# Kernel tuning notes

Measured on AMD Instinct MI355X. Metric: run time of the kernel, lower is better.

The kernel has to match this reference:

```python
import jax, jax.numpy as jnp
import numpy as np

B, H, W = 1024, 66, 64
N = 62          # EEG channels / graph nodes
TOPK = 62       # hardcoded in Network
NUM_CLASSES = 3


def setup_inputs() -> dict:
    key = jax.random.key(0)
    ks = jax.random.split(key, 17)
    p = lambda i, s: (jax.random.normal(ks[i], s, jnp.float32) * 0.05)
    return {
        "x": jax.random.normal(ks[0], (B, H, W), jnp.float32),
        "conv_w": p(1, (32, 1, 5, 5)), "conv_b": p(2, (32,)),
        "s1_bn_w": p(3, (480, 64)), "s1_bn_b": p(4, (64,)),
        "s1_g_w": p(5, (480, 32)), "s1_g_b": p(6, (32,)),
        "s2_bn_w": p(7, (32, 64)), "s2_bn_b": p(8, (64,)),
        "s2_g_w": p(9, (32, 32)), "s2_g_b": p(10, (32,)),
        "s3_bn_w": p(11, (32, 64)), "s3_bn_b": p(12, (64,)),
        "s3_g_w": p(13, (32, 32)), "s3_g_b": p(14, (32,)),
        "fc_w": p(15, (620, NUM_CLASSES)), "fc_b": p(16, (NUM_CLASSES,)),
    }


def _maxpool_last(x, k):
    # MaxPool over the last dim with kernel=stride=k, VALID (floor) semantics.
    win = (1,) * (x.ndim - 1) + (k,)
    return jax.lax.reduce_window(x, -jnp.inf, jax.lax.max, win, win, "VALID")


def _sogc(x, bn_w, bn_b, g_w, g_b):
    # x: (Bg, N, F). Self-organized graph construction + DenseGCNConv.
    Bg = x.shape[0]
    xa = jnp.tanh(x @ bn_w + bn_b)                     # (Bg, N, bn)
    adj = jax.nn.softmax(jnp.einsum("bnf,bmf->bnm", xa, xa), axis=2)
    # topk mask per row (scatter of ones at top-k column indices)
    _, idx = jax.lax.top_k(adj, TOPK)                  # (Bg, N, k)
    bi = jnp.arange(Bg)[:, None, None]
    ri = jnp.arange(N)[None, :, None]
    mask = jnp.zeros_like(adj).at[bi, ri, idx].set(1.0)
    adj = adj * mask
    # SOGC adds eye, then DenseGCNConv(add_loop=True) overwrites diag with 1
    d = jnp.arange(N)
    adj = adj.at[:, d, d].set(1.0)
    # symmetric degree normalization with clamp(min=1)
    deg_is = jnp.clip(adj.sum(-1), 1.0, None) ** -0.5  # (Bg, N)
    adj = deg_is[:, :, None] * adj * deg_is[:, None, :]
    return jnp.einsum("bnm,bmo->bno", adj, x @ g_w) + g_b


def reference(x, conv_w, conv_b, s1_bn_w, s1_bn_b, s1_g_w, s1_g_b,
              s2_bn_w, s2_bn_b, s2_g_w, s2_g_b,
              s3_bn_w, s3_bn_b, s3_g_w, s3_g_b, fc_w, fc_b):
    b = x.shape[0]
    h = jax.lax.conv_general_dilated(
        x[:, None], conv_w, (1, 1), "VALID",
        dimension_numbers=("NCHW", "OIHW", "NCHW"))
    h = jax.nn.relu(h + conv_b[None, :, None, None])   # (B,32,62,60)
    h = _maxpool_last(h, 4)                            # (B,32,62,15)
    h = h.reshape(b, -1, 480)                          # (B,62,480)
    h = _sogc(h.reshape(-1, N, 480), s1_bn_w, s1_bn_b, s1_g_w, s1_g_b)
    h = _sogc(h.reshape(-1, N, 32), s2_bn_w, s2_bn_b, s2_g_w, s2_g_b)
    h = _sogc(h.reshape(-1, N, 32), s3_bn_w, s3_bn_b, s3_g_w, s3_g_b)
    h = _maxpool_last(h, 3)                            # (B,62,10)
    h = h.reshape(h.shape[0], -1)                      # (B,620) — adapted head
    return h @ fc_w + fc_b                             # (B,3)
```

## Files before the change

### kernel.cpp

```cpp
#include <hip/hip_runtime.h>
#include <math.h>


typedef _Float16 f16x8 __attribute__((ext_vector_type(8)));
typedef float    f32x4  __attribute__((ext_vector_type(4)));
typedef float    f32x16 __attribute__((ext_vector_type(16)));

__device__ __forceinline__ unsigned short f32_to_f16u(float f) {
    const _Float16 h = (_Float16)f;
    return __builtin_bit_cast(unsigned short, h);
}
__device__ __forceinline__ float f16u_to_f32(unsigned short u) {
    return (float)__builtin_bit_cast(_Float16, u);
}
__device__ __forceinline__ float fast_tanh(float v) {
    v = fminf(fmaxf(v, -15.f), 15.f);
    const float ex = __expf(2.f * v);
    return (ex - 1.f) / (ex + 1.f);
}


__global__ __launch_bounds__(256) void prepack_kernel(
    const float* __restrict__ bnw1, const float* __restrict__ gw1,
    const float* __restrict__ cw,
    const float* __restrict__ bnw2, const float* __restrict__ gw2,
    const float* __restrict__ bnw3, const float* __restrict__ gw3,
    unsigned short* __restrict__ wp)
{
    const int idx = blockIdx.x * 256 + threadIdx.x;
    if (idx < 49152) {
        const int kc = idx / 3072, r = idx - kc * 3072;
        const int q = r / 768, r2 = r - q * 768;
        const int col = r2 >> 3, j = r2 & 7;
        float w = 0.f;
        if (kc < 15) {
            const int s = q * 8 + j;
            const int ko = s * 15 + kc;
            w = (col < 64) ? bnw1[ko * 64 + col] : gw1[ko * 32 + (col - 64)];
        }
        wp[idx] = f32_to_f16u(w);
    } else if (idx >= 92160 && idx < 93696) {
        const int e = idx - 92160;
        const int c = e >> 9, l = (e >> 3) & 63, j = e & 7;
        const int ch = l & 31, dio = l >> 5;
        const int di = (c < 2) ? (2 * c + dio) : (4 + dio);
        const float w = (j < 5 && di < 5) ? cw[ch * 25 + di * 5 + j] : 0.f;
        wp[idx] = f32_to_f16u(w);
    } else if (idx >= 94208 && idx < 100352) {
        const int e2 = idx - 94208;
        const int s = e2 / 3072, r = e2 - s * 3072;
        const int col = r >> 5, k = r & 31;
        const float* bnw = s ? bnw3 : bnw2;
        const float* gw  = s ? gw3  : gw2;
        const float w = (col < 64) ? bnw[k * 64 + col] : gw[k * 32 + (col - 64)];
        wp[idx] = f32_to_f16u(w);
    }
}

__global__ __launch_bounds__(256, 4) void mega_kernel(
    const float* __restrict__ x,
    const float* __restrict__ cb,
    const unsigned short* __restrict__ wp,
    const float* __restrict__ bnb1,  const float* __restrict__ gb1,
    const float* __restrict__ bnb2,  const float* __restrict__ gb2,
    const float* __restrict__ bnb3,  const float* __restrict__ gb3,
    const float* __restrict__ fcw,   const float* __restrict__ fcb,
    float* __restrict__ out)
{
    __shared__ __align__(16) char lds[28416];
    unsigned short* xb   = (unsigned short*)lds;
    unsigned short* Xcol = (unsigned short*)(lds + 10880);
    unsigned short* xaH  = (unsigned short*)lds;
    unsigned short* zB   = xaH + 4608;
    unsigned short* P    = xaH + 6912;
    unsigned short* xB   = xaH + 11520;
    float* degis = (float*)(lds + 28160);

    const int b = blockIdx.x;
    const int tid = threadIdx.x;
    const int wv = tid >> 6, ln = tid & 63;

    const float4* xg = (const float4*)(x + (size_t)b * 4224);
    for (int idx = tid; idx < 1056; idx += 256) {
        const float4 v = xg[idx];
        const int row = idx >> 4, c4 = idx & 15;
        short4 s;
        s.x = (short)f32_to_f16u(v.x);
        s.y = (short)f32_to_f16u(v.y);
        s.z = (short)f32_to_f16u(v.z);
        s.w = (short)f32_to_f16u(v.w);
        *(short4*)(xb + row * 80 + c4 * 4) = s;
    }
    for (int idx = tid; idx < 544; idx += 256) {
        const int row = idx >> 3, w = idx & 7;
        ((unsigned int*)(xb + row * 80 + 64))[w] = 0u;
    }
    if (tid < 64) {
        const int row = 66 + (tid >> 5), w = tid & 31;
        ((unsigned int*)(xb + row * 80))[w] = 0u;
    }
    if (tid < 128)
        ((unsigned int*)(Xcol + 62 * 128))[tid] = 0u;
    __syncthreads();

    const int m = ln & 15, rp = (ln >> 4) & 1, dio = ln >> 5;
    const int ch = ln & 31, hi = ln >> 5;
    f16x8 Wc[3];
    #pragma unroll
    for (int c = 0; c < 3; ++c)
        Wc[c] = *(const f16x8*)(wp + 92160 + c * 512 + ln * 8);
    const float cbv = cb[ch];
    const f32x16 z16 = {};

    const int rt = ln & 15, q = ln >> 4;
    f32x4 acc[6];
    #pragma unroll
    for (int nt = 0; nt < 6; ++nt) acc[nt] = (f32x4){0.f, 0.f, 0.f, 0.f};

    for (int pjg = 0; pjg < 4; ++pjg) {
        const int j0 = pjg * 16;
        f16x8 Bp[6];
        {
            const unsigned short* wB = wp + (pjg * 4) * 3072 + q * 768 + rt * 8;
            #pragma unroll
            for (int nt = 0; nt < 6; ++nt) Bp[nt] = *(const f16x8*)(wB + nt * 128);
        }
        #pragma unroll 4
        for (int p = wv; p < 31; p += 4) {
            const int r0 = 2 * p;
            const unsigned short* base = xb + (r0 + rp + dio) * 80 + j0 + m;
            f32x16 a32;
            #pragma unroll
            for (int c = 0; c < 3; ++c) {
                const f16x8 Af = *(const f16x8*)(base + c * 160);
                a32 = __builtin_amdgcn_mfma_f32_32x32x16_f16(
                          Af, Wc[c], (c == 0) ? z16 : a32, 0, 0, 0);
            }
            #pragma unroll
            for (int i = 0; i < 4; ++i) {
                const int t = 2 * i + hi;
                const int rpo = t >> 2, g = t & 3;
                float v = fmaxf(fmaxf(a32[4 * i], a32[4 * i + 1]),
                                fmaxf(a32[4 * i + 2], a32[4 * i + 3])) + cbv;
                v = fmaxf(v, 0.f);
                if (!(pjg == 3 && g == 3)) {
                    const int row = r0 + rpo;
                    const int tt = ch * 62 + row;
                    const int n = tt >> 5, sf = tt & 31;
                    Xcol[n * 128 + ((g * 32 + sf) ^ ((n & 7) << 3))] =
                        f32_to_f16u(v);
                }
            }
        }
        __syncthreads();
        {
            const int row = wv * 16 + rt;
            #pragma unroll
            for (int g = 0; g < 4; ++g) {
                f16x8 Bn[6];
                #pragma unroll
                for (int nt = 0; nt < 6; ++nt)
                    Bn[nt] = (g < 3)
                        ? *(const f16x8*)(wp + (pjg * 4 + g + 1) * 3072
                                          + q * 768 + nt * 128 + rt * 8)
                        : Bp[nt];
                const f16x8 A = *(const f16x8*)(
                    Xcol + row * 128 + (((g * 4 + q) ^ (row & 7)) << 3));
                #pragma unroll
                for (int nt = 0; nt < 6; ++nt)
                    acc[nt] = __builtin_amdgcn_mfma_f32_16x16x32_f16(A, Bp[nt], acc[nt], 0, 0, 0);
                #pragma unroll
                for (int nt = 0; nt < 6; ++nt) Bp[nt] = Bn[nt];
            }
        }
        __syncthreads();
    }

    {
        const int rq = wv * 4 + q;
        #pragma unroll
        for (int nt = 0; nt < 4; ++nt) {
            const float bb = bnb1[nt * 16 + rt];
            #pragma unroll
            for (int j = 0; j < 4; ++j) {
                const int r = rq * 4 + j;
                float th = fast_tanh(acc[nt][j] + bb);
                if (r >= 62) th = 0.f;
                xaH[r * 72 + nt * 16 + rt] = f32_to_f16u(th);
            }
        }
        #pragma unroll
        for (int nt = 4; nt < 6; ++nt) {
            const int o = (nt - 4) * 16 + rt;
            unsigned short zv[4];
            #pragma unroll
            for (int j = 0; j < 4; ++j) {
                const int r = rq * 4 + j;
                zv[j] = (r < 62) ? f32_to_f16u(acc[nt][j]) : (unsigned short)0;
            }
            *(ushort4*)(zB + o * 72 + rq * 4) =
                make_ushort4(zv[0], zv[1], zv[2], zv[3]);
        }
    }
    __syncthreads();

    const int c16 = ln & 15;
    const int r62 = wv * 16 + c16;
    const unsigned short* wstg = wp + 94208;

    #pragma unroll 1
    for (int st = 0; st < 3; ++st) {
        f16x8 zPre[2][2];
        #pragma unroll
        for (int kh = 0; kh < 2; ++kh) {
            const int chh = (kh * 4 + q) * 8;
            zPre[kh][0] = *(const f16x8*)(zB + c16 * 72 + chh);
            zPre[kh][1] = *(const f16x8*)(zB + (16 + c16) * 72 + chh);
        }
        f32x4 sacc[4];
        #pragma unroll
        for (int ct = 0; ct < 4; ++ct) sacc[ct] = (f32x4){0.f, 0.f, 0.f, 0.f};
        const int arow = r62 * 72;
        #pragma unroll
        for (int kh = 0; kh < 2; ++kh) {
            const int chh = (kh * 4 + q) * 8;
            const f16x8 Bw = *(const f16x8*)(xaH + arow + chh);
            #pragma unroll
            for (int ct = 0; ct < 4; ++ct) {
                const f16x8 Act = *(const f16x8*)(xaH + (ct * 16 + c16) * 72 + chh);
                sacc[ct] = __builtin_amdgcn_mfma_f32_16x16x32_f16(Act, Bw, sacc[ct], 0, 0, 0);
            }
        }
        f16x8 wbPre[6];
        if (st < 2) {
            const unsigned short* wsB = wstg + st * 3072;
            #pragma unroll
            for (int nt = 0; nt < 6; ++nt)
                wbPre[nt] = *(const f16x8*)(wsB + (nt * 16 + c16) * 32 + q * 8);
        }
        float mx = -1e30f;
        #pragma unroll
        for (int ct = 0; ct < 4; ++ct)
            #pragma unroll
            for (int j = 0; j < 4; ++j) mx = fmaxf(mx, sacc[ct][j]);
        mx = fmaxf(mx, __shfl_xor(mx, 16));
        mx = fmaxf(mx, __shfl_xor(mx, 32));
        float e[4][4];
        float sum = 0.f;
        #pragma unroll
        for (int ct = 0; ct < 4; ++ct)
            #pragma unroll
            for (int j = 0; j < 4; ++j) {
                float v = __expf(sacc[ct][j] - mx);
                if (ct == 3 && j >= 2 && q == 3) v = 0.f;
                e[ct][j] = v; sum += v;
            }
        sum += __shfl_xor(sum, 16);
        sum += __shfl_xor(sum, 32);
        const float inv = 1.f / sum;
        #pragma unroll
        for (int ct = 0; ct < 4; ++ct)
            #pragma unroll
            for (int j = 0; j < 4; ++j) e[ct][j] *= inv;
        if (r62 < 62 && q == (c16 >> 2)) {
            #pragma unroll
            for (int ct = 0; ct < 4; ++ct)
                if (ct == wv) {
                    #pragma unroll
                    for (int j = 0; j < 4; ++j)
                        if (j == (c16 & 3)) e[ct][j] = 1.f;
                }
        }
        float dg = 0.f;
        #pragma unroll
        for (int ct = 0; ct < 4; ++ct)
            #pragma unroll
            for (int j = 0; j < 4; ++j) dg += e[ct][j];
        dg += __shfl_xor(dg, 16);
        dg += __shfl_xor(dg, 32);
        float dri = rsqrtf(fmaxf(dg, 1.f));
        if (r62 >= 62) dri = 1.f;
        if (q == 0) degis[r62] = dri;
        __syncthreads();
        {
            unsigned short* pr = P + r62 * 72 + q * 4;
            if (r62 < 62) {
                #pragma unroll
                for (int ct = 0; ct < 4; ++ct) {
                    const float4 dm = *(const float4*)(degis + ct * 16 + q * 4);
                    ushort4 pv;
                    pv.x = f32_to_f16u(e[ct][0] * dri * dm.x);
                    pv.y = f32_to_f16u(e[ct][1] * dri * dm.y);
                    pv.z = f32_to_f16u(e[ct][2] * dri * dm.z);
                    pv.w = f32_to_f16u(e[ct][3] * dri * dm.w);
                    *(ushort4*)(pr + ct * 16) = pv;
                }
            } else {
                #pragma unroll
                for (int ct = 0; ct < 4; ++ct)
                    *(ushort4*)(pr + ct * 16) = make_ushort4(0, 0, 0, 0);
            }
        }
        __syncthreads();
        {
            f32x4 oa0 = {0.f, 0.f, 0.f, 0.f}, oa1 = {0.f, 0.f, 0.f, 0.f};
            #pragma unroll
            for (int kh = 0; kh < 2; ++kh) {
                const int chh = (kh * 4 + q) * 8;
                const f16x8 pa = *(const f16x8*)(P + (wv * 16 + c16) * 72 + chh);
                oa0 = __builtin_amdgcn_mfma_f32_16x16x32_f16(pa, zPre[kh][0], oa0, 0, 0, 0);
                oa1 = __builtin_amdgcn_mfma_f32_16x16x32_f16(pa, zPre[kh][1], oa1, 0, 0, 0);
            }
            const float* gbp = (st == 0) ? gb1 : (st == 1) ? gb2 : gb3;
            const float g0 = gbp[c16], g1 = gbp[16 + c16];
            #pragma unroll
            for (int j = 0; j < 4; ++j) {
                const int n = wv * 16 + q * 4 + j;
                unsigned short* xr = xB + n * 40 + c16;
                if (n < 62) {
                    xr[0]  = f32_to_f16u(oa0[j] + g0);
                    xr[16] = f32_to_f16u(oa1[j] + g1);
                } else { xr[0] = 0; xr[16] = 0; }
            }
        }
        __syncthreads();
        if (st == 2) break;

        {
            const float* bnbp = (st == 0) ? bnb2 : bnb3;
            const f16x8 ax = *(const f16x8*)(xB + (wv * 16 + c16) * 40 + q * 8);
            f32x4 sa[6];
            #pragma unroll
            for (int nt = 0; nt < 6; ++nt) {
                f32x4 zz = {0.f, 0.f, 0.f, 0.f};
                sa[nt] = __builtin_amdgcn_mfma_f32_16x16x32_f16(ax, wbPre[nt], zz, 0, 0, 0);
            }
            #pragma unroll
            for (int nt = 0; nt < 4; ++nt) {
                const float bb = bnbp[nt * 16 + c16];
                #pragma unroll
                for (int j = 0; j < 4; ++j) {
                    const int n = wv * 16 + q * 4 + j;
                    float th = fast_tanh(sa[nt][j] + bb);
                    if (n >= 62) th = 0.f;
                    xaH[n * 72 + nt * 16 + c16] = f32_to_f16u(th);
                }
            }
            #pragma unroll
            for (int nt = 4; nt < 6; ++nt) {
                const int o = (nt - 4) * 16 + c16;
                unsigned short zv[4];
                #pragma unroll
                for (int j = 0; j < 4; ++j) {
                    const int n = wv * 16 + q * 4 + j;
                    zv[j] = (n < 62) ? f32_to_f16u(sa[nt][j]) : (unsigned short)0;
                }
                *(ushort4*)(zB + o * 72 + wv * 16 + q * 4) =
                    make_ushort4(zv[0], zv[1], zv[2], zv[3]);
            }
        }
        __syncthreads();
    }

    float a0 = 0.f, a1 = 0.f, a2 = 0.f;
    for (int t = tid; t < 620; t += 256) {
        const int n = t / 10, tt = t - (t / 10) * 10;
        const unsigned short* pr = xB + n * 40 + tt * 3;
        const float p = fmaxf(fmaxf(f16u_to_f32(pr[0]), f16u_to_f32(pr[1])),
                              f16u_to_f32(pr[2]));
        const float* fw = fcw + t * 3;
        a0 = fmaf(p, fw[0], a0);
        a1 = fmaf(p, fw[1], a1);
        a2 = fmaf(p, fw[2], a2);
    }
    #pragma unroll
    for (int off = 32; off; off >>= 1) {
        a0 += __shfl_down(a0, off);
        a1 += __shfl_down(a1, off);
        a2 += __shfl_down(a2, off);
    }
    float* red = degis;
    if (ln == 0) { red[wv * 3 + 0] = a0; red[wv * 3 + 1] = a1; red[wv * 3 + 2] = a2; }
    __syncthreads();
    if (tid == 0) {
        out[b * 3 + 0] = red[0] + red[3] + red[6] + red[9]  + fcb[0];
        out[b * 3 + 1] = red[1] + red[4] + red[7] + red[10] + fcb[1];
        out[b * 3 + 2] = red[2] + red[5] + red[8] + red[11] + fcb[2];
    }
}

extern "C" void kernel_launch(void* const* d_in, const int* in_sizes, int n_in,
                              void* d_out, int out_size, void* d_ws, size_t ws_size,
                              hipStream_t stream) {
    const float* x     = (const float*)d_in[0];
    const float* convw = (const float*)d_in[1];
    const float* convb = (const float*)d_in[2];
    const float* bnw1  = (const float*)d_in[3];
    const float* bnb1  = (const float*)d_in[4];
    const float* gw1   = (const float*)d_in[5];
    const float* gb1   = (const float*)d_in[6];
    const float* bnw2  = (const float*)d_in[7];
    const float* bnb2  = (const float*)d_in[8];
    const float* gw2   = (const float*)d_in[9];
    const float* gb2   = (const float*)d_in[10];
    const float* bnw3  = (const float*)d_in[11];
    const float* bnb3  = (const float*)d_in[12];
    const float* gw3   = (const float*)d_in[13];
    const float* gb3   = (const float*)d_in[14];
    const float* fcw   = (const float*)d_in[15];
    const float* fcb   = (const float*)d_in[16];

    unsigned short* wp = (unsigned short*)d_ws;

    prepack_kernel<<<392, 256, 0, stream>>>(bnw1, gw1, convw, bnw2, gw2,
                                            bnw3, gw3, wp);
    mega_kernel<<<1024, 256, 0, stream>>>(x, convb, wp, bnb1, gb1,
                                          bnb2, gb2, bnb3, gb3,
                                          fcw, fcb, (float*)d_out);
}
```

Baseline: 73.52 us.

## Split fused kernel into two-way conv/GEMM partials plus separate SOGC tail kernel

The single per-sample mega kernel is split in two. A conv+first-GEMM kernel runs 2048 blocks, each handling half of the input columns (split-K), and writes fp32 partial accumulators to workspace. A second kernel sums the two partials and runs the SOGC stages and head. The intent is more parallelism and higher occupancy (launch bounds raised to 7, smaller LDS) in the conv stage, at the cost of a global round trip for the partials and an extra launch.

New measurement: 91.80 us. +24.9%, slower.

```diff
diff --git a/kernel.cpp b/kernel.cpp
--- a/kernel.cpp
+++ b/kernel.cpp
@@ -19,6 +19,7 @@
     return (ex - 1.f) / (ex + 1.f);
 }
 
+#define PART_OFF 204800
 
 __global__ __launch_bounds__(256) void prepack_kernel(
     const float* __restrict__ bnw1, const float* __restrict__ gw1,
@@ -57,47 +58,34 @@
     }
 }
 
-__global__ __launch_bounds__(256, 4) void mega_kernel(
+__global__ __launch_bounds__(256, 7) void conv_g1_kernel(
     const float* __restrict__ x,
     const float* __restrict__ cb,
     const unsigned short* __restrict__ wp,
-    const float* __restrict__ bnb1,  const float* __restrict__ gb1,
-    const float* __restrict__ bnb2,  const float* __restrict__ gb2,
-    const float* __restrict__ bnb3,  const float* __restrict__ gb3,
-    const float* __restrict__ fcw,   const float* __restrict__ fcb,
-    float* __restrict__ out)
+    float4* __restrict__ part)
 {
-    __shared__ __align__(16) char lds[28416];
-    unsigned short* xb   = (unsigned short*)lds;
-    unsigned short* Xcol = (unsigned short*)(lds + 10880);
-    unsigned short* xaH  = (unsigned short*)lds;
-    unsigned short* zB   = xaH + 4608;
-    unsigned short* P    = xaH + 6912;
-    unsigned short* xB   = xaH + 11520;
-    float* degis = (float*)(lds + 28160);
-
-    const int b = blockIdx.x;
+    __shared__ __align__(16) char lds[21824];
+    unsigned short* xbs  = (unsigned short*)lds;
+    unsigned short* Xcol = (unsigned short*)(lds + 5440);
+
+    const int bx = blockIdx.x;
+    const int b = bx >> 1, h = bx & 1;
     const int tid = threadIdx.x;
     const int wv = tid >> 6, ln = tid & 63;
 
-    const float4* xg = (const float4*)(x + (size_t)b * 4224);
-    for (int idx = tid; idx < 1056; idx += 256) {
-        const float4 v = xg[idx];
-        const int row = idx >> 4, c4 = idx & 15;
+    const float* xgf = x + (size_t)b * 4224;
+    for (int idx = tid; idx < 680; idx += 256) {
+        const int row = idx / 10, c4 = idx - (idx / 10) * 10;
+        const int col = h * 32 + c4 * 4;
         short4 s;
-        s.x = (short)f32_to_f16u(v.x);
-        s.y = (short)f32_to_f16u(v.y);
-        s.z = (short)f32_to_f16u(v.z);
-        s.w = (short)f32_to_f16u(v.w);
-        *(short4*)(xb + row * 80 + c4 * 4) = s;
-    }
-    for (int idx = tid; idx < 544; idx += 256) {
-        const int row = idx >> 3, w = idx & 7;
-        ((unsigned int*)(xb + row * 80 + 64))[w] = 0u;
-    }
-    if (tid < 64) {
-        const int row = 66 + (tid >> 5), w = tid & 31;
-        ((unsigned int*)(xb + row * 80))[w] = 0u;
+        if (row < 66 && col < 64) {
+            const float4 v = *(const float4*)(xgf + row * 64 + col);
+            s.x = (short)f32_to_f16u(v.x);
+            s.y = (short)f32_to_f16u(v.y);
+            s.z = (short)f32_to_f16u(v.z);
+            s.w = (short)f32_to_f16u(v.w);
+        } else { s.x = 0; s.y = 0; s.z = 0; s.w = 0; }
+        *(short4*)(xbs + row * 40 + c4 * 4) = s;
     }
     if (tid < 128)
         ((unsigned int*)(Xcol + 62 * 128))[tid] = 0u;
@@ -117,8 +105,9 @@
     #pragma unroll
     for (int nt = 0; nt < 6; ++nt) acc[nt] = (f32x4){0.f, 0.f, 0.f, 0.f};
 
-    for (int pjg = 0; pjg < 4; ++pjg) {
-        const int j0 = pjg * 16;
+    for (int pp = 0; pp < 2; ++pp) {
+        const int pjg = h * 2 + pp;
+        const int j0s = pp * 16;
         f16x8 Bp[6];
         {
             const unsigned short* wB = wp + (pjg * 4) * 3072 + q * 768 + rt * 8;
@@ -128,11 +117,11 @@
         #pragma unroll 4
         for (int p = wv; p < 31; p += 4) {
             const int r0 = 2 * p;
-            const unsigned short* base = xb + (r0 + rp + dio) * 80 + j0 + m;
+            const unsigned short* base = xbs + (r0 + rp + dio) * 40 + j0s + m;
             f32x16 a32;
             #pragma unroll
             for (int c = 0; c < 3; ++c) {
-                const f16x8 Af = *(const f16x8*)(base + c * 160);
+                const f16x8 Af = *(const f16x8*)(base + c * 80);
                 a32 = __builtin_amdgcn_mfma_f32_32x32x16_f16(
                           Af, Wc[c], (c == 0) ? z16 : a32, 0, 0, 0);
             }
@@ -140,16 +129,14 @@
             for (int i = 0; i < 4; ++i) {
                 const int t = 2 * i + hi;
                 const int rpo = t >> 2, g = t & 3;
-                float v = fmaxf(fmaxf(a32[4 * i], a32[4 * i + 1]),
-                                fmaxf(a32[4 * i + 2], a32[4 * i + 3])) + cbv;
-                v = fmaxf(v, 0.f);
-                if (!(pjg == 3 && g == 3)) {
-                    const int row = r0 + rpo;
-                    const int tt = ch * 62 + row;
-                    const int n = tt >> 5, sf = tt & 31;
-                    Xcol[n * 128 + ((g * 32 + sf) ^ ((n & 7) << 3))] =
-                        f32_to_f16u(v);
-                }
+                float v = fmaxf(fmaxf(fmaxf(fmaxf(
+                              a32[4 * i], a32[4 * i + 1]), a32[4 * i + 2]),
+                              a32[4 * i + 3]) + cbv, 0.f);
+                const int row = r0 + rpo;
+                const int tt = ch * 62 + row;
+                const int n = tt >> 5, sf = tt & 31;
+                Xcol[n * 128 + ((g * 32 + sf) ^ ((n & 7) << 3))] =
+                    f32_to_f16u(v);
             }
         }
         __syncthreads();
@@ -174,6 +161,52 @@
             }
         }
         __syncthreads();
+    }
+
+    {
+        float4* dst = part + (size_t)bx * 1536;
+        #pragma unroll
+        for (int nt = 0; nt < 6; ++nt) {
+            float4 v;
+            v.x = acc[nt][0]; v.y = acc[nt][1];
+            v.z = acc[nt][2]; v.w = acc[nt][3];
+            dst[nt * 256 + tid] = v;
+        }
+    }
+}
+
+__global__ __launch_bounds__(256, 4) void sogc_tail_kernel(
+    const unsigned short* __restrict__ wp,
+    const float4* __restrict__ part,
+    const float* __restrict__ bnb1,  const float* __restrict__ gb1,
+    const float* __restrict__ gb2,   const float* __restrict__ gb3,
+    const float* __restrict__ bnb2,  const float* __restrict__ bnb3,
+    const float* __restrict__ fcw,   const float* __restrict__ fcb,
+    float* __restrict__ out)
+{
+    __shared__ __align__(16) char lds[28416];
+    unsigned short* xaH  = (unsigned short*)lds;
+    unsigned short* zB   = xaH + 4608;
+    unsigned short* P    = xaH + 6912;
+    unsigned short* xB   = xaH + 11520;
+    float* degis = (float*)(lds + 28160);
+
+    const int b = blockIdx.x;
+    const int tid = threadIdx.x;
+    const int wv = tid >> 6, ln = tid & 63;
+    const int rt = ln & 15, q = ln >> 4;
+
+    f32x4 acc[6];
+    {
+        const float4* p0 = part + (size_t)(b * 2) * 1536;
+        const float4* p1 = p0 + 1536;
+        #pragma unroll
+        for (int nt = 0; nt < 6; ++nt) {
+            const float4 a = p0[nt * 256 + tid];
+            const float4 c = p1[nt * 256 + tid];
+            acc[nt][0] = a.x + c.x; acc[nt][1] = a.y + c.y;
+            acc[nt][2] = a.z + c.z; acc[nt][3] = a.w + c.w;
+        }
     }
 
     {
@@ -307,7 +340,7 @@
             #pragma unroll
             for (int kh = 0; kh < 2; ++kh) {
                 const int chh = (kh * 4 + q) * 8;
-                const f16x8 pa = *(const f16x8*)(P + (wv * 16 + c16) * 72 + chh);
+                const f16x8 pa = *(const f16x8*)(P + r62 * 72 + chh);
                 oa0 = __builtin_amdgcn_mfma_f32_16x16x32_f16(pa, zPre[kh][0], oa0, 0, 0, 0);
                 oa1 = __builtin_amdgcn_mfma_f32_16x16x32_f16(pa, zPre[kh][1], oa1, 0, 0, 0);
             }
@@ -328,7 +361,7 @@
 
         {
             const float* bnbp = (st == 0) ? bnb2 : bnb3;
-            const f16x8 ax = *(const f16x8*)(xB + (wv * 16 + c16) * 40 + q * 8);
+            const f16x8 ax = *(const f16x8*)(xB + r62 * 40 + q * 8);
             f32x4 sa[6];
             #pragma unroll
             for (int nt = 0; nt < 6; ++nt) {
@@ -411,10 +444,12 @@
     const float* fcb   = (const float*)d_in[16];
 
     unsigned short* wp = (unsigned short*)d_ws;
+    float4* part = (float4*)((char*)d_ws + PART_OFF);
 
     prepack_kernel<<<392, 256, 0, stream>>>(bnw1, gw1, convw, bnw2, gw2,
                                             bnw3, gw3, wp);
-    mega_kernel<<<1024, 256, 0, stream>>>(x, convb, wp, bnb1, gb1,
-                                          bnb2, gb2, bnb3, gb3,
-                                          fcw, fcb, (float*)d_out);
-}
+    conv_g1_kernel<<<2048, 256, 0, stream>>>(x, convb, wp, part);
+    sogc_tail_kernel<<<1024, 256, 0, stream>>>(wp, part, bnb1, gb1, gb2, gb3,
+                                               bnb2, bnb3, fcw, fcb,
+                                               (float*)d_out);
+}
```
